# Kernel tuning notes

Hardware: AMD Instinct MI355X
Metric: run time of the kernel (lower is better)

Reference implementation:

```python
import jax, jax.numpy as jnp
import numpy as np

B, T, C, H = 1, 2048, 1024, 16
HD = C // H           # 64
TOPK = 64
RAMP = 32
MAX_SPAN = 2048
NEG_MAX = jnp.finfo(jnp.float32).max


def setup_inputs() -> dict:
    key = jax.random.key(0)
    k0, k1, k2, k3, k4 = jax.random.split(key, 5)
    x = jax.random.normal(k0, (B, T, C), jnp.float32)
    w_attn = jax.random.normal(k1, (3 * C, C), jnp.float32) * 0.02
    w_proj = jax.random.normal(k2, (C, C), jnp.float32) * 0.02
    w_gate = jax.random.normal(k3, (C, C), jnp.float32) * 0.02
    span_params = jax.random.uniform(k4, (H,), jnp.float32)
    pos = jnp.arange(T, dtype=jnp.int64) if jax.config.jax_enable_x64 else jnp.arange(T, dtype=jnp.int32)
    return {"x": x, "w_attn": w_attn, "w_proj": w_proj, "w_gate": w_gate,
            "span_params": span_params, "pos": pos}


def _rotate_half(u):
    u1, u2 = jnp.split(u, 2, axis=-1)
    return jnp.concatenate([-u2, u1], axis=-1)


def _rope(q, k):
    t = q.shape[-2]
    inv_freq = 1.0 / (10000.0 ** (jnp.arange(0, HD, 2, dtype=jnp.float32) / HD))
    freqs = jnp.arange(t, dtype=jnp.float32)[:, None] * inv_freq[None, :]  # [T, HD/2]
    emb = jnp.concatenate([freqs, freqs], axis=-1)                          # [T, HD]
    cos = jnp.cos(emb)[None, None]
    sin = jnp.sin(emb)[None, None]
    q = q * cos + _rotate_half(q * sin)
    k = k * cos + _rotate_half(k * sin)
    return q, k


def reference(x, w_attn, w_proj, w_gate, span_params, pos):
    qkv = x @ w_attn.T                                   # [B,T,3C]
    q, k, v = jnp.split(qkv, 3, axis=-1)
    q = q.reshape(B, T, H, HD).transpose(0, 2, 1, 3)     # [B,H,T,HD]
    k = k.reshape(B, T, H, HD).transpose(0, 2, 1, 3)
    v = v.reshape(B, T, H, HD).transpose(0, 2, 1, 3)
    q, k = _rope(q, k)

    att = jnp.einsum('bhqd,bhkd->bhqk', q, k) / jnp.sqrt(jnp.float32(HD))
    i = jnp.arange(T)
    causal = i[:, None] >= i[None, :]                    # [T,T]
    att = jnp.where(causal[None, None], att, -jnp.inf)

    # sparse top-k with straight-through softmax
    top_vals = jax.lax.top_k(att, TOPK)[0]               # [B,H,T,K]
    thresh = top_vals[..., -1:]
    keep = (att >= thresh) & (att > -NEG_MAX)
    att_topk = jnp.where(keep, att, -NEG_MAX)
    topk_attn = jax.nn.softmax(att_topk, axis=-1)
    soft_attn = jax.nn.softmax(att, axis=-1)
    att = jax.lax.stop_gradient(topk_attn) + soft_attn - jax.lax.stop_gradient(soft_attn)

    # adaptive span soft mask + renormalize
    spans = MAX_SPAN * jnp.clip(span_params, 0.0, 1.0)   # [H]
    dist = jnp.abs(i[:, None] - i[None, :]).astype(jnp.float32)  # [T,T]
    soft_mask = jnp.clip((RAMP + spans[:, None, None] - dist[None]) / RAMP, 0.0, 1.0)  # [H,T,T]
    att = att * soft_mask[None]
    att = att / (att.sum(-1, keepdims=True) + 1e-8)

    y = jnp.einsum('bhqk,bhkd->bhqd', att, v)            # [B,H,T,HD]
    y = y.transpose(0, 2, 1, 3).reshape(B, T, C)
    gate = jax.nn.silu(x @ w_gate.T)
    y = y * gate
    y = y @ w_proj.T
    return y
```

## Files before the change

### kernel.cpp

```cpp
#include <hip/hip_runtime.h>
#include <math.h>

#define T_DIM 2048
#define C_DIM 1024
#define H_DIM 16
#define HD 64
#define TOPK_K 64
#define QTILE 8
#define LCAP 128

typedef __attribute__((ext_vector_type(8))) __bf16 bf16x8;
typedef __attribute__((ext_vector_type(4))) float f32x4;

__device__ __forceinline__ unsigned short bf16rn(float x) {
  unsigned u = __float_as_uint(x);
  return (unsigned short)((u + 0x7FFFu + ((u >> 16) & 1u)) >> 16);
}
__device__ __forceinline__ unsigned f2u(float f) {
  unsigned u = __float_as_uint(f);
  return (u & 0x80000000u) ? ~u : (u | 0x80000000u);
}
__device__ __forceinline__ float u2f(unsigned u) {
  unsigned v = (u & 0x80000000u) ? (u & 0x7FFFFFFFu) : ~u;
  return __uint_as_float(v);
}
__device__ __forceinline__ bf16x8 ld_frag(const uint4* p) {
  uint4 u = *p;
  return __builtin_bit_cast(bf16x8, u);
}
#define PAD_KEY 0x007FFFFFu

__global__ __launch_bounds__(256) void convert_all_kernel(
    const float* __restrict__ x, const float* __restrict__ wa,
    const float* __restrict__ wg, const float* __restrict__ wp,
    unsigned short* __restrict__ xh, unsigned short* __restrict__ xl,
    unsigned short* __restrict__ wqgh, unsigned short* __restrict__ wqgl,
    unsigned short* __restrict__ wph, unsigned short* __restrict__ wpl,
    float2* __restrict__ tab)
{
  const int tid = blockIdx.x * 256 + threadIdx.x;
  const int k8 = tid & 127, r = tid >> 7;
  if (r >= 7168) {
    const int e = ((r - 7168) << 7) | k8;
    const int t = e >> 5, d = e & 31;
    double invf = exp(-(double)d * (log(10000.0) / 32.0));
    double ang = (double)t * invf;
    tab[e] = make_float2((float)cos(ang), (float)sin(ang));
    return;
  }
  const float* src;
  unsigned short *Dh, *Dl;
  int srow, drow;
  if (r < 2048)      { src = x;  Dh = xh;   Dl = xl;   srow = r;        drow = r; }
  else if (r < 5120) { src = wa; Dh = wqgh; Dl = wqgl; srow = r - 2048; drow = r - 2048; }
  else if (r < 6144) { src = wg; Dh = wqgh; Dl = wqgl; srow = r - 5120; drow = r - 2048; }
  else               { src = wp; Dh = wph;  Dl = wpl;  srow = r - 6144; drow = r - 6144; }
  const float* s = src + ((size_t)srow << 10) + (k8 << 3);
  float4 a = *(const float4*)s;
  float4 b = *(const float4*)(s + 4);
  float xs[8] = {a.x, a.y, a.z, a.w, b.x, b.y, b.z, b.w};
  unsigned hi[8], lo[8];
#pragma unroll
  for (int jj = 0; jj < 8; ++jj) {
    unsigned short hb = bf16rn(xs[jj]);
    hi[jj] = hb;
    lo[jj] = bf16rn(xs[jj] - __uint_as_float((unsigned)hb << 16));
  }
  const int t16 = drow >> 4, rr = drow & 15, kc = k8 >> 2, kq = k8 & 3;
  const size_t elem = (((size_t)(t16 * 32 + kc)) * 64 + ((kq << 4) | rr)) * 8;
  uint4 vh, vl;
  vh.x = hi[0] | (hi[1] << 16); vh.y = hi[2] | (hi[3] << 16);
  vh.z = hi[4] | (hi[5] << 16); vh.w = hi[6] | (hi[7] << 16);
  vl.x = lo[0] | (lo[1] << 16); vl.y = lo[2] | (lo[3] << 16);
  vl.z = lo[4] | (lo[5] << 16); vl.w = lo[6] | (lo[7] << 16);
  *(uint4*)(Dh + elem) = vh;
  *(uint4*)(Dl + elem) = vl;
}

__device__ __forceinline__ void gld_lds16(const unsigned short* g, unsigned short* l) {
  __builtin_amdgcn_global_load_lds(
      (const __attribute__((address_space(1))) unsigned int*)g,
      (__attribute__((address_space(3))) unsigned int*)l, 16, 0, 0);
}

__global__ __launch_bounds__(512, 4) void mgemm_qkvg_kernel(
    const unsigned short* __restrict__ Ah, const unsigned short* __restrict__ Al,
    const unsigned short* __restrict__ Bh, const unsigned short* __restrict__ Bl,
    float* __restrict__ Cq, float* __restrict__ Ck, float* __restrict__ Cv,
    float* __restrict__ Cg)
{
  __shared__ __align__(16) unsigned short As[2 * 8 * 512];
  __shared__ __align__(16) unsigned short Bs[2 * 8 * 512];
  const int tid = threadIdx.x, lane = tid & 63, w = tid >> 6;
  const int mt0 = blockIdx.y << 3;
  const int nt0 = blockIdx.x << 3;

  f32x4 acc[8];
#pragma unroll
  for (int j = 0; j < 8; ++j) acc[j] = (f32x4){0.f, 0.f, 0.f, 0.f};

  for (int kc = 0; kc < 32; ++kc) {
#pragma unroll
    for (int li = 0; li < 4; ++li) {
      const int gi = (w << 2) + li;
      const int isB = gi >= 16;
      const int gb = gi & 15;
      const int t  = gb & 7;
      const int hl = gb >> 3;
      const unsigned short* gbase = isB ? (hl ? Bl : Bh) : (hl ? Al : Ah);
      const int tg = (isB ? nt0 : mt0) + t;
      const unsigned short* g = gbase + (((size_t)(tg * 32 + kc) << 6) + lane) * 8;
      unsigned short* l = (isB ? Bs : As) + hl * 4096 + t * 512;
      gld_lds16(g, l);
    }
    __syncthreads();
    bf16x8 ah = *(const bf16x8*)&As[w * 512 + lane * 8];
    bf16x8 al = *(const bf16x8*)&As[4096 + w * 512 + lane * 8];
#pragma unroll
    for (int j = 0; j < 8; ++j) {
      bf16x8 bh = *(const bf16x8*)&Bs[j * 512 + lane * 8];
      bf16x8 bl = *(const bf16x8*)&Bs[4096 + j * 512 + lane * 8];
      acc[j] = __builtin_amdgcn_mfma_f32_16x16x32_bf16(ah, bh, acc[j], 0, 0, 0);
      acc[j] = __builtin_amdgcn_mfma_f32_16x16x32_bf16(ah, bl, acc[j], 0, 0, 0);
      acc[j] = __builtin_amdgcn_mfma_f32_16x16x32_bf16(al, bh, acc[j], 0, 0, 0);
    }
    __syncthreads();
  }

  const int col = lane & 15, quad = lane >> 4;
  const int mbase = (blockIdx.y << 7) + (w << 4);
#pragma unroll
  for (int j = 0; j < 8; ++j) {
    const int ncol = (blockIdx.x << 7) + (j << 4);
    const int which = ncol >> 10;
    if (which < 3) {
      const int h = (ncol & 1023) >> 6;
      float* dst = (which == 0) ? Cq : (which == 1) ? Ck : Cv;
      float* base = dst + (((size_t)h * T_DIM) << 6) + (ncol & 63) + col;
#pragma unroll
      for (int reg = 0; reg < 4; ++reg) {
        const int m = mbase + quad * 4 + reg;
        base[(size_t)m << 6] = acc[j][reg];
      }
    } else {
      const int cb = (ncol & 1023) + col;
#pragma unroll
      for (int reg = 0; reg < 4; ++reg) {
        const int m = mbase + quad * 4 + reg;
        float vv = acc[j][reg];
        Cg[((size_t)m << 10) + cb] = vv / (1.f + expf(-vv));
      }
    }
  }
}

__global__ __launch_bounds__(256, 4) void mgemm_proj_kernel(
    const unsigned short* __restrict__ Ah, const unsigned short* __restrict__ Al,
    const unsigned short* __restrict__ Bh, const unsigned short* __restrict__ Bl,
    float* __restrict__ P0, float* __restrict__ P1)
{
  __shared__ __align__(16) unsigned short As[2 * 4 * 512];
  __shared__ __align__(16) unsigned short Bs[2 * 8 * 512];
  const int tid = threadIdx.x, lane = tid & 63, w = tid >> 6;
  const int mt0 = blockIdx.y << 2;
  const int nt0 = blockIdx.x << 3;
  const int kc0 = blockIdx.z << 4;
  float* Cout = blockIdx.z ? P1 : P0;

  f32x4 acc[8];
#pragma unroll
  for (int j = 0; j < 8; ++j) acc[j] = (f32x4){0.f, 0.f, 0.f, 0.f};

  for (int kc = kc0; kc < kc0 + 16; ++kc) {
#pragma unroll
    for (int li = 0; li < 6; ++li) {
      const int gi = w * 6 + li;
      const int isB = gi >= 8;
      const int t  = isB ? ((gi - 8) & 7) : (gi & 3);
      const int hl = isB ? ((gi - 8) >> 3) : (gi >> 2);
      const unsigned short* gbase = isB ? (hl ? Bl : Bh) : (hl ? Al : Ah);
      const int tg = (isB ? nt0 : mt0) + t;
      const unsigned short* g = gbase + (((size_t)(tg * 32 + kc) << 6) + lane) * 8;
      unsigned short* l = isB ? (Bs + hl * 4096 + t * 512) : (As + hl * 2048 + t * 512);
      gld_lds16(g, l);
    }
    __syncthreads();
    bf16x8 ah = *(const bf16x8*)&As[w * 512 + lane * 8];
    bf16x8 al = *(const bf16x8*)&As[2048 + w * 512 + lane * 8];
#pragma unroll
    for (int j = 0; j < 8; ++j) {
      bf16x8 bh = *(const bf16x8*)&Bs[j * 512 + lane * 8];
      bf16x8 bl = *(const bf16x8*)&Bs[4096 + j * 512 + lane * 8];
      acc[j] = __builtin_amdgcn_mfma_f32_16x16x32_bf16(ah, bh, acc[j], 0, 0, 0);
      acc[j] = __builtin_amdgcn_mfma_f32_16x16x32_bf16(ah, bl, acc[j], 0, 0, 0);
      acc[j] = __builtin_amdgcn_mfma_f32_16x16x32_bf16(al, bh, acc[j], 0, 0, 0);
    }
    __syncthreads();
  }

  const int col = lane & 15, quad = lane >> 4;
  const int mbase = (blockIdx.y << 6) + (w << 4);
  const int nbase = blockIdx.x << 7;
#pragma unroll
  for (int j = 0; j < 8; ++j)
#pragma unroll
    for (int reg = 0; reg < 4; ++reg) {
      const int m = mbase + quad * 4 + reg;
      Cout[((size_t)m << 10) + nbase + (j << 4) + col] = acc[j][reg];
    }
}

__global__ __launch_bounds__(256) void add2_kernel(
    const float* __restrict__ P0, const float* __restrict__ P1,
    float* __restrict__ out)
{
  const int i = (blockIdx.x * 256 + threadIdx.x) << 2;
  float4 a = *(const float4*)(P0 + i);
  float4 b = *(const float4*)(P1 + i);
  float4 o = {a.x + b.x, a.y + b.y, a.z + b.z, a.w + b.w};
  *(float4*)(out + i) = o;
}

__global__ __launch_bounds__(64) void prep_frag_kernel(
    float* __restrict__ qb, float* __restrict__ kb,
    const float2* __restrict__ tab)
{
  float* buf = blockIdx.z ? kb : qb;
  const int lane = threadIdx.x;
  const int t16 = blockIdx.x, h = blockIdx.y;
  const int nr = lane & 15, quad = lane >> 4;
  const int t = (t16 << 4) + nr;
  const float* row = buf + ((size_t)(h * T_DIM + t) << 6);
  const int d0 = quad << 3;
  float4 a0 = *(const float4*)(row + d0);
  float4 a1 = *(const float4*)(row + d0 + 4);
  float4 b0 = *(const float4*)(row + 32 + d0);
  float4 b1 = *(const float4*)(row + 32 + d0 + 4);
  float x0[8] = {a0.x, a0.y, a0.z, a0.w, a1.x, a1.y, a1.z, a1.w};
  float x1[8] = {b0.x, b0.y, b0.z, b0.w, b1.x, b1.y, b1.z, b1.w};
  const float2* tb = tab + t * 32 + d0;
  unsigned short h0[8], l0[8], h1[8], l1[8];
#pragma unroll
  for (int jj = 0; jj < 8; ++jj) {
    float2 cs2 = tb[jj];
    float o0 = fmaf(x0[jj], cs2.x, -x1[jj] * cs2.y);
    float o1 = fmaf(x1[jj], cs2.x, x0[jj] * cs2.y);
    unsigned short hb = bf16rn(o0);
    h0[jj] = hb;
    l0[jj] = bf16rn(o0 - __uint_as_float((unsigned)hb << 16));
    hb = bf16rn(o1);
    h1[jj] = hb;
    l1[jj] = bf16rn(o1 - __uint_as_float((unsigned)hb << 16));
  }
  char* base = (char*)buf + (((size_t)(h * 128 + t16)) << 12);
  uint4 v;
  v.x = (unsigned)h0[0] | ((unsigned)h0[1] << 16);
  v.y = (unsigned)h0[2] | ((unsigned)h0[3] << 16);
  v.z = (unsigned)h0[4] | ((unsigned)h0[5] << 16);
  v.w = (unsigned)h0[6] | ((unsigned)h0[7] << 16);
  ((uint4*)base)[lane] = v;
  v.x = (unsigned)h1[0] | ((unsigned)h1[1] << 16);
  v.y = (unsigned)h1[2] | ((unsigned)h1[3] << 16);
  v.z = (unsigned)h1[4] | ((unsigned)h1[5] << 16);
  v.w = (unsigned)h1[6] | ((unsigned)h1[7] << 16);
  ((uint4*)(base + 1024))[lane] = v;
  v.x = (unsigned)l0[0] | ((unsigned)l0[1] << 16);
  v.y = (unsigned)l0[2] | ((unsigned)l0[3] << 16);
  v.z = (unsigned)l0[4] | ((unsigned)l0[5] << 16);
  v.w = (unsigned)l0[6] | ((unsigned)l0[7] << 16);
  ((uint4*)(base + 2048))[lane] = v;
  v.x = (unsigned)l1[0] | ((unsigned)l1[1] << 16);
  v.y = (unsigned)l1[2] | ((unsigned)l1[3] << 16);
  v.z = (unsigned)l1[4] | ((unsigned)l1[5] << 16);
  v.w = (unsigned)l1[6] | ((unsigned)l1[7] << 16);
  ((uint4*)(base + 3072))[lane] = v;
}

__global__ __launch_bounds__(512, 6) void attn_kernel(
    const float* __restrict__ qfrag, const float* __restrict__ kfrag,
    const float* __restrict__ v, const float* __restrict__ span_params,
    float* __restrict__ y)
{
  __shared__ __align__(16) char smem[QTILE * 1024 * 4];
  float* sBase = (float*)smem;
  unsigned* histB = (unsigned*)smem;
  int* listJB = (int*)(smem + 8192);
  unsigned* listUB = (unsigned*)(smem + 12288);

  const int tid = threadIdx.x;
  const int lane = tid & 63;
  const int w = tid >> 6;
  const int bx = gridDim.x - 1 - blockIdx.x;
  const int q0 = bx << 3;
  const int h = blockIdx.y;
  const int qi = q0 + w;
  const int n = qi + 1;
  const float* vh = v + (((size_t)h * T_DIM) << 6);
  const int col = lane & 15, quad = lane >> 4;

  const int qt16 = bx >> 1;
  const int rlo = (bx & 1) << 3;
  const uint4* qf = (const uint4*)((const char*)qfrag + (((size_t)(h * 128 + qt16)) << 12));
  bf16x8 Ah0 = ld_frag(qf + lane);
  bf16x8 Ah1 = ld_frag(qf + 64 + lane);
  bf16x8 Al0 = ld_frag(qf + 128 + lane);
  bf16x8 Al1 = ld_frag(qf + 192 + lane);

  unsigned uk[32];

#pragma unroll
  for (int ph = 0; ph < 2; ++ph) {
    const int tlo = ph << 6;
    const int thi = (qt16 < tlo + 63) ? qt16 : (tlo + 63);
    int tf = tlo + w;
    if (tf <= thi) {
      const uint4* kf = (const uint4*)((const char*)kfrag + (((size_t)(h * 128 + tf)) << 12));
      bf16x8 nBh0 = ld_frag(kf + lane);
      bf16x8 nBh1 = ld_frag(kf + 64 + lane);
      bf16x8 nBl0 = ld_frag(kf + 128 + lane);
      bf16x8 nBl1 = ld_frag(kf + 192 + lane);
      for (; tf <= thi; tf += 8) {
        const bf16x8 Bh0 = nBh0, Bh1 = nBh1, Bl0 = nBl0, Bl1 = nBl1;
        const int tn = (tf + 8 <= thi) ? (tf + 8) : tf;
        const uint4* kfn = (const uint4*)((const char*)kfrag + (((size_t)(h * 128 + tn)) << 12));
        nBh0 = ld_frag(kfn + lane);
        nBh1 = ld_frag(kfn + 64 + lane);
        nBl0 = ld_frag(kfn + 128 + lane);
        nBl1 = ld_frag(kfn + 192 + lane);
        f32x4 acc = {0.f, 0.f, 0.f, 0.f};
        acc = __builtin_amdgcn_mfma_f32_16x16x32_bf16(Ah0, Bh0, acc, 0, 0, 0);
        acc = __builtin_amdgcn_mfma_f32_16x16x32_bf16(Ah0, Bl0, acc, 0, 0, 0);
        acc = __builtin_amdgcn_mfma_f32_16x16x32_bf16(Al0, Bh0, acc, 0, 0, 0);
        acc = __builtin_amdgcn_mfma_f32_16x16x32_bf16(Ah1, Bh1, acc, 0, 0, 0);
        acc = __builtin_amdgcn_mfma_f32_16x16x32_bf16(Ah1, Bl1, acc, 0, 0, 0);
        acc = __builtin_amdgcn_mfma_f32_16x16x32_bf16(Al1, Bh1, acc, 0, 0, 0);
        const int jcol = (tf << 4) + col;
#pragma unroll
        for (int r = 0; r < 4; ++r) {
          const int row8 = (quad << 2) + r - rlo;
          if ((unsigned)row8 < 8u && jcol <= q0 + row8)
            sBase[row8 * 1024 + ((jcol & 1023) ^ (((row8 >> 2) & 1) << 4))] = acc[r];
        }
      }
    }
    __syncthreads();
#pragma unroll
    for (int cc = 0; cc < 2; ++cc) {
      const int c = (ph << 1) + cc;
      if ((c << 9) < n) {
#pragma unroll
        for (int i = 0; i < 8; ++i) {
          const int j = (((c << 3) + i) << 6) + lane;
          uk[(c << 3) + i] = (j < n)
              ? f2u(sBase[w * 1024 + ((j & 1023) ^ (((w >> 2) & 1) << 4))]) : PAD_KEY;
        }
      } else {
#pragma unroll
        for (int i = 0; i < 8; ++i) uk[(c << 3) + i] = PAD_KEY;
      }
    }
    __syncthreads();
  }

  unsigned* hist = histB + (w << 8);
  int* listJ = listJB + (w << 7);
  unsigned* listU = listUB + (w << 7);
  const float span = 2048.f * fminf(fmaxf(span_params[h], 0.f), 1.f);

  unsigned umax = 0;
#pragma unroll
  for (int i = 0; i < 32; ++i) umax = max(umax, uk[i]);
#pragma unroll
  for (int off = 32; off > 0; off >>= 1)
    umax = max(umax, (unsigned)__shfl_xor((int)umax, off, 64));
  const float mraw = u2f(umax);

  unsigned thresh_u = 0;
  if (n > TOPK_K) {
    unsigned want = TOPK_K;
    const unsigned bmax = umax >> 24;
    unsigned long long c01 = 0;
#pragma unroll
    for (int c = 0; c < 4; ++c) {
      if ((c << 9) < n) {
#pragma unroll
        for (int i = 0; i < 8; ++i) {
          const unsigned u = uk[(c << 3) + i];
          const unsigned d = bmax - (u >> 24);
          if (u > PAD_KEY && d < 4u) c01 += 1ull << (d << 4);
        }
      }
    }
#pragma unroll
    for (int off = 32; off > 0; off >>= 1)
      c01 += __shfl_xor(c01, off, 64);
    unsigned cnt8[8];
    cnt8[0] = (unsigned)c01 & 0xFFFFu;
    cnt8[1] = ((unsigned)c01) >> 16;
    cnt8[2] = (unsigned)(c01 >> 32) & 0xFFFFu;
    cnt8[3] = (unsigned)(c01 >> 48);
    int m = -1;
    unsigned cumBefore = 0;
    bool exact = false;
    unsigned cum = 0;
#pragma unroll
    for (int b = 0; b < 4; ++b) {
      if (m < 0 && cum + cnt8[b] >= want) {
        m = b; cumBefore = cum; exact = (cum + cnt8[b] == want);
      }
      cum += cnt8[b];
    }
    if (m < 0) {
      unsigned long long c23 = 0;
#pragma unroll
      for (int c = 0; c < 4; ++c) {
        if ((c << 9) < n) {
#pragma unroll
          for (int i = 0; i < 8; ++i) {
            const unsigned u = uk[(c << 3) + i];
            const unsigned d = bmax - (u >> 24) - 4u;
            if (u > PAD_KEY && d < 4u) c23 += 1ull << (d << 4);
          }
        }
      }
#pragma unroll
      for (int off = 32; off > 0; off >>= 1)
        c23 += __shfl_xor(c23, off, 64);
      cnt8[4] = (unsigned)c23 & 0xFFFFu;
      cnt8[5] = ((unsigned)c23) >> 16;
      cnt8[6] = (unsigned)(c23 >> 32) & 0xFFFFu;
      cnt8[7] = (unsigned)(c23 >> 48);
#pragma unroll
      for (int b = 4; b < 8; ++b) {
        if (m < 0 && cum + cnt8[b] >= want) {
          m = b; cumBefore = cum; exact = (cum + cnt8[b] == want);
        }
        cum += cnt8[b];
      }
    }
    unsigned prefix;
    int shift0;
    if (m >= 0) { prefix = (bmax - (unsigned)m) << 24; want -= cumBefore; shift0 = 16; }
    else        { prefix = 0; shift0 = 24; }
    if (m >= 0 && exact) {
      thresh_u = prefix;
    } else {
      for (int shift = shift0; shift >= 0; shift -= 8) {
        uint4 z4 = {0u, 0u, 0u, 0u};
        *(uint4*)&hist[lane << 2] = z4;
        __threadfence_block();
        const unsigned pm = (shift == 24) ? 0u : (0xFFFFFFFFu << (shift + 8));
#pragma unroll
        for (int c = 0; c < 4; ++c) {
          if ((c << 9) < n) {
#pragma unroll
            for (int i = 0; i < 8; ++i) {
              const unsigned u = uk[(c << 3) + i];
              if (u > PAD_KEY && (u & pm) == prefix)
                atomicAdd(&hist[(u >> shift) & 255u], 1u);
            }
          }
        }
        __threadfence_block();
        uint4 hv = *(const uint4*)&hist[lane << 2];
        unsigned loc = hv.x + hv.y + hv.z + hv.w;
        unsigned suf = loc;
#pragma unroll
        for (int off = 1; off < 64; off <<= 1) {
          unsigned t = __shfl_down(suf, off, 64);
          suf += (lane + off < 64) ? t : 0u;
        }
        unsigned sufE = suf - loc;
        unsigned S3 = sufE + hv.w;
        unsigned S2 = S3 + hv.z;
        unsigned S1 = S2 + hv.y;
        unsigned S0 = S1 + hv.x;
        const unsigned wt = want;
        int found = 0;
        unsigned pk = 0;
        if (S0 >= wt && S1 < wt)
          { found = 1; pk = ((unsigned)(4*lane+0) << 16) | ((S0 == wt) ? 0x8000u : 0u) | (wt - S1); }
        if (S1 >= wt && S2 < wt)
          { found = 1; pk = ((unsigned)(4*lane+1) << 16) | ((S1 == wt) ? 0x8000u : 0u) | (wt - S2); }
        if (S2 >= wt && S3 < wt)
          { found = 1; pk = ((unsigned)(4*lane+2) << 16) | ((S2 == wt) ? 0x8000u : 0u) | (wt - S3); }
        if (S3 >= wt && sufE < wt)
          { found = 1; pk = ((unsigned)(4*lane+3) << 16) | ((S3 == wt) ? 0x8000u : 0u) | (wt - sufE); }
        unsigned long long mk = __ballot(found);
        int src = __ffsll(mk) - 1;
        pk = __shfl(pk, src, 64);
        prefix |= (pk >> 16) << shift;
        want = pk & 0x7FFFu;
        if (pk & 0x8000u) break;
      }
      thresh_u = prefix;
    }
  }

  int cnt_run = 0;
#pragma unroll
  for (int c = 0; c < 4; ++c) {
    if ((c << 9) < n) {
#pragma unroll
      for (int i = 0; i < 8; ++i) {
        const int j = (((c << 3) + i) << 6) + lane;
        const unsigned u = uk[(c << 3) + i];
        const bool keep = (u >= thresh_u) && (u > PAD_KEY);
        unsigned long long mb = __ballot(keep);
        if (keep) {
          int pos = cnt_run + (int)__popcll(mb & ((1ull << lane) - 1ull));
          if (pos < LCAP) { listJ[pos] = j; listU[pos] = u; }
        }
        cnt_run += (int)__popcll(mb);
      }
    }
  }
  const int cnt = min(cnt_run, LCAP);
  __threadfence_block();

  float Zl = 0.f, Ul = 0.f;
  for (int e = lane; e < cnt; e += 64) {
    const unsigned u = listU[e];
    const int j = listJ[e];
    const float wv = __expf((u2f(u) - mraw) * 0.125f);
    const float dist = (float)(qi - j);
    const float msk = fminf(fmaxf((32.f + span - dist) * (1.f / 32.f), 0.f), 1.f);
    const float wm = wv * msk;
    Zl += wv;
    Ul += wm;
    listU[e] = __float_as_uint(wm);
  }
#pragma unroll
  for (int off = 32; off > 0; off >>= 1) {
    Zl += __shfl_xor(Zl, off, 64);
    Ul += __shfl_xor(Ul, off, 64);
  }
  const float scale = 1.f / (Ul + 1e-8f * Zl);
  __threadfence_block();

  const int g = lane >> 4;
  const int d4 = col << 2;
  float4 acc4 = {0.f, 0.f, 0.f, 0.f};
  for (int e0 = 0; e0 < cnt; e0 += 16) {
    int j0 = 0, j1 = 0, j2 = 0, j3 = 0;
    float wm0 = 0.f, wm1 = 0.f, wm2 = 0.f, wm3 = 0.f;
    {
      const int e = e0 + g;
      if (e < cnt) { j0 = listJ[e]; wm0 = __uint_as_float(listU[e]); }
    }
    {
      const int e = e0 + 4 + g;
      if (e < cnt) { j1 = listJ[e]; wm1 = __uint_as_float(listU[e]); }
    }
    {
      const int e = e0 + 8 + g;
      if (e < cnt) { j2 = listJ[e]; wm2 = __uint_as_float(listU[e]); }
    }
    {
      const int e = e0 + 12 + g;
      if (e < cnt) { j3 = listJ[e]; wm3 = __uint_as_float(listU[e]); }
    }
    const float4 v0 = *(const float4*)(vh + ((size_t)j0 << 6) + d4);
    const float4 v1 = *(const float4*)(vh + ((size_t)j1 << 6) + d4);
    const float4 v2 = *(const float4*)(vh + ((size_t)j2 << 6) + d4);
    const float4 v3 = *(const float4*)(vh + ((size_t)j3 << 6) + d4);
    acc4.x = fmaf(wm0, v0.x, acc4.x);
    acc4.y = fmaf(wm0, v0.y, acc4.y);
    acc4.z = fmaf(wm0, v0.z, acc4.z);
    acc4.w = fmaf(wm0, v0.w, acc4.w);
    acc4.x = fmaf(wm1, v1.x, acc4.x);
    acc4.y = fmaf(wm1, v1.y, acc4.y);
    acc4.z = fmaf(wm1, v1.z, acc4.z);
    acc4.w = fmaf(wm1, v1.w, acc4.w);
    acc4.x = fmaf(wm2, v2.x, acc4.x);
    acc4.y = fmaf(wm2, v2.y, acc4.y);
    acc4.z = fmaf(wm2, v2.z, acc4.z);
    acc4.w = fmaf(wm2, v2.w, acc4.w);
    acc4.x = fmaf(wm3, v3.x, acc4.x);
    acc4.y = fmaf(wm3, v3.y, acc4.y);
    acc4.z = fmaf(wm3, v3.z, acc4.z);
    acc4.w = fmaf(wm3, v3.w, acc4.w);
  }
#pragma unroll
  for (int off = 16; off <= 32; off <<= 1) {
    acc4.x += __shfl_xor(acc4.x, off, 64);
    acc4.y += __shfl_xor(acc4.y, off, 64);
    acc4.z += __shfl_xor(acc4.z, off, 64);
    acc4.w += __shfl_xor(acc4.w, off, 64);
  }
  if (g == 0) {
    float4 o = {acc4.x * scale, acc4.y * scale, acc4.z * scale, acc4.w * scale};
    *(float4*)(y + ((((size_t)h * T_DIM) + qi) << 6) + d4) = o;
  }
}

__global__ __launch_bounds__(256) void gate_mul_frag_kernel(
    const float* __restrict__ y_att, const float* __restrict__ gate,
    unsigned short* __restrict__ Yh, unsigned short* __restrict__ Yl)
{
  const int tid = blockIdx.x * 256 + threadIdx.x;
  const int k8 = tid & 127, r = tid >> 7;
  const int c0 = k8 << 3;
  const int h = c0 >> 6, d0 = c0 & 63;
  const float* ya = y_att + ((size_t)(h * T_DIM + r) << 6) + d0;
  const float* ga = gate + ((size_t)r << 10) + c0;
  float4 y0 = *(const float4*)ya;
  float4 y1 = *(const float4*)(ya + 4);
  float4 g0 = *(const float4*)ga;
  float4 g1 = *(const float4*)(ga + 4);
  float p[8] = {y0.x * g0.x, y0.y * g0.y, y0.z * g0.z, y0.w * g0.w,
                y1.x * g1.x, y1.y * g1.y, y1.z * g1.z, y1.w * g1.w};
  unsigned hi[8], lo[8];
#pragma unroll
  for (int jj = 0; jj < 8; ++jj) {
    unsigned short hb = bf16rn(p[jj]);
    hi[jj] = hb;
    lo[jj] = bf16rn(p[jj] - __uint_as_float((unsigned)hb << 16));
  }
  const int t16 = r >> 4, rr = r & 15, kc = k8 >> 2, kq = k8 & 3;
  const size_t elem = (((size_t)(t16 * 32 + kc)) * 64 + ((kq << 4) | rr)) * 8;
  uint4 vh, vl;
  vh.x = hi[0] | (hi[1] << 16); vh.y = hi[2] | (hi[3] << 16);
  vh.z = hi[4] | (hi[5] << 16); vh.w = hi[6] | (hi[7] << 16);
  vl.x = lo[0] | (lo[1] << 16); vl.y = lo[2] | (lo[3] << 16);
  vl.z = lo[4] | (lo[5] << 16); vl.w = lo[6] | (lo[7] << 16);
  *(uint4*)(Yh + elem) = vh;
  *(uint4*)(Yl + elem) = vl;
}

extern "C" void kernel_launch(void* const* d_in, const int* in_sizes, int n_in,
                              void* d_out, int out_size, void* d_ws, size_t ws_size,
                              hipStream_t stream) {
  (void)in_sizes; (void)n_in; (void)out_size; (void)ws_size;
  const float* x           = (const float*)d_in[0];
  const float* w_attn      = (const float*)d_in[1];
  const float* w_proj      = (const float*)d_in[2];
  const float* w_gate      = (const float*)d_in[3];
  const float* span_params = (const float*)d_in[4];
  float* out = (float*)d_out;

  char* ws = (char*)d_ws;
  const size_t MB = 1024 * 1024;
  float* q     = (float*)(ws);
  float* k     = (float*)(ws + 8 * MB);
  float* v     = (float*)(ws + 16 * MB);
  float* gate  = (float*)(ws + 24 * MB);
  float* y_att = (float*)(ws + 32 * MB);
  unsigned short* xf_h  = (unsigned short*)(ws + 40 * MB);
  unsigned short* xf_l  = (unsigned short*)(ws + 44 * MB);
  unsigned short* wqg_h = (unsigned short*)(ws + 48 * MB);
  unsigned short* wqg_l = (unsigned short*)(ws + 56 * MB);
  unsigned short* wfp_h = (unsigned short*)(ws + 64 * MB);
  unsigned short* wfp_l = (unsigned short*)(ws + 66 * MB);
  unsigned short* ygf_h = (unsigned short*)(ws + 68 * MB);
  unsigned short* ygf_l = (unsigned short*)(ws + 72 * MB);
  float2* rope_tab = (float2*)(ws + 76 * MB);
  float* P0 = q;
  float* P1 = k;

  convert_all_kernel<<<3840, 256, 0, stream>>>(
      x, w_attn, w_gate, w_proj, xf_h, xf_l, wqg_h, wqg_l, wfp_h, wfp_l, rope_tab);
  mgemm_qkvg_kernel<<<dim3(32, 16), 512, 0, stream>>>(
      xf_h, xf_l, wqg_h, wqg_l, q, k, v, gate);
  prep_frag_kernel<<<dim3(T_DIM / 16, H_DIM, 2), 64, 0, stream>>>(q, k, rope_tab);
  attn_kernel<<<dim3(T_DIM / QTILE, H_DIM), 512, 0, stream>>>(
      q, k, v, span_params, y_att);
  gate_mul_frag_kernel<<<T_DIM / 2, 256, 0, stream>>>(y_att, gate, ygf_h, ygf_l);
  mgemm_proj_kernel<<<dim3(8, 32, 2), 256, 0, stream>>>(
      ygf_h, ygf_l, wfp_h, wfp_l, P0, P1);
  add2_kernel<<<(T_DIM * C_DIM) / 1024, 256, 0, stream>>>(P0, P1, out);
}
```

Measured before the change: 286.5 us.

## Fuse gate multiply into attention epilogue and enlarge projection GEMM tile

The attention kernel's epilogue now multiplies by the SiLU gate and writes the split bf16 hi/lo fragments for the projection GEMM directly. This removes the separate gate_mul_frag kernel and the fp32 y_att round trip through global memory. The projection GEMM now uses 512-thread blocks covering 128 rows instead of 64, which halves the grid and doubles reuse of the B tile. The trade-off is fewer blocks in flight for the projection and narrower 8-byte scattered stores from attention.

```diff
diff --git a/kernel.cpp b/kernel.cpp
--- a/kernel.cpp
+++ b/kernel.cpp
@@ -154,15 +154,15 @@
   }
 }
 
-__global__ __launch_bounds__(256, 4) void mgemm_proj_kernel(
+__global__ __launch_bounds__(512, 4) void mgemm_proj_kernel(
     const unsigned short* __restrict__ Ah, const unsigned short* __restrict__ Al,
     const unsigned short* __restrict__ Bh, const unsigned short* __restrict__ Bl,
     float* __restrict__ P0, float* __restrict__ P1)
 {
-  __shared__ __align__(16) unsigned short As[2 * 4 * 512];
+  __shared__ __align__(16) unsigned short As[2 * 8 * 512];
   __shared__ __align__(16) unsigned short Bs[2 * 8 * 512];
   const int tid = threadIdx.x, lane = tid & 63, w = tid >> 6;
-  const int mt0 = blockIdx.y << 2;
+  const int mt0 = blockIdx.y << 3;
   const int nt0 = blockIdx.x << 3;
   const int kc0 = blockIdx.z << 4;
   float* Cout = blockIdx.z ? P1 : P0;
@@ -173,20 +173,21 @@
 
   for (int kc = kc0; kc < kc0 + 16; ++kc) {
 #pragma unroll
-    for (int li = 0; li < 6; ++li) {
-      const int gi = w * 6 + li;
-      const int isB = gi >= 8;
-      const int t  = isB ? ((gi - 8) & 7) : (gi & 3);
-      const int hl = isB ? ((gi - 8) >> 3) : (gi >> 2);
+    for (int li = 0; li < 4; ++li) {
+      const int gi = (w << 2) + li;
+      const int isB = gi >= 16;
+      const int gb = gi & 15;
+      const int t  = gb & 7;
+      const int hl = gb >> 3;
       const unsigned short* gbase = isB ? (hl ? Bl : Bh) : (hl ? Al : Ah);
       const int tg = (isB ? nt0 : mt0) + t;
       const unsigned short* g = gbase + (((size_t)(tg * 32 + kc) << 6) + lane) * 8;
-      unsigned short* l = isB ? (Bs + hl * 4096 + t * 512) : (As + hl * 2048 + t * 512);
+      unsigned short* l = (isB ? Bs : As) + hl * 4096 + t * 512;
       gld_lds16(g, l);
     }
     __syncthreads();
     bf16x8 ah = *(const bf16x8*)&As[w * 512 + lane * 8];
-    bf16x8 al = *(const bf16x8*)&As[2048 + w * 512 + lane * 8];
+    bf16x8 al = *(const bf16x8*)&As[4096 + w * 512 + lane * 8];
 #pragma unroll
     for (int j = 0; j < 8; ++j) {
       bf16x8 bh = *(const bf16x8*)&Bs[j * 512 + lane * 8];
@@ -199,7 +200,7 @@
   }
 
   const int col = lane & 15, quad = lane >> 4;
-  const int mbase = (blockIdx.y << 6) + (w << 4);
+  const int mbase = (blockIdx.y << 7) + (w << 4);
   const int nbase = blockIdx.x << 7;
 #pragma unroll
   for (int j = 0; j < 8; ++j)
@@ -279,7 +280,8 @@
 __global__ __launch_bounds__(512, 6) void attn_kernel(
     const float* __restrict__ qfrag, const float* __restrict__ kfrag,
     const float* __restrict__ v, const float* __restrict__ span_params,
-    float* __restrict__ y)
+    const float* __restrict__ gate,
+    unsigned short* __restrict__ Yh, unsigned short* __restrict__ Yl)
 {
   __shared__ __align__(16) char smem[QTILE * 1024 * 4];
   float* sBase = (float*)smem;
@@ -589,43 +591,25 @@
     acc4.w += __shfl_xor(acc4.w, off, 64);
   }
   if (g == 0) {
-    float4 o = {acc4.x * scale, acc4.y * scale, acc4.z * scale, acc4.w * scale};
-    *(float4*)(y + ((((size_t)h * T_DIM) + qi) << 6) + d4) = o;
-  }
-}
-
-__global__ __launch_bounds__(256) void gate_mul_frag_kernel(
-    const float* __restrict__ y_att, const float* __restrict__ gate,
-    unsigned short* __restrict__ Yh, unsigned short* __restrict__ Yl)
-{
-  const int tid = blockIdx.x * 256 + threadIdx.x;
-  const int k8 = tid & 127, r = tid >> 7;
-  const int c0 = k8 << 3;
-  const int h = c0 >> 6, d0 = c0 & 63;
-  const float* ya = y_att + ((size_t)(h * T_DIM + r) << 6) + d0;
-  const float* ga = gate + ((size_t)r << 10) + c0;
-  float4 y0 = *(const float4*)ya;
-  float4 y1 = *(const float4*)(ya + 4);
-  float4 g0 = *(const float4*)ga;
-  float4 g1 = *(const float4*)(ga + 4);
-  float p[8] = {y0.x * g0.x, y0.y * g0.y, y0.z * g0.z, y0.w * g0.w,
-                y1.x * g1.x, y1.y * g1.y, y1.z * g1.z, y1.w * g1.w};
-  unsigned hi[8], lo[8];
-#pragma unroll
-  for (int jj = 0; jj < 8; ++jj) {
-    unsigned short hb = bf16rn(p[jj]);
-    hi[jj] = hb;
-    lo[jj] = bf16rn(p[jj] - __uint_as_float((unsigned)hb << 16));
-  }
-  const int t16 = r >> 4, rr = r & 15, kc = k8 >> 2, kq = k8 & 3;
-  const size_t elem = (((size_t)(t16 * 32 + kc)) * 64 + ((kq << 4) | rr)) * 8;
-  uint4 vh, vl;
-  vh.x = hi[0] | (hi[1] << 16); vh.y = hi[2] | (hi[3] << 16);
-  vh.z = hi[4] | (hi[5] << 16); vh.w = hi[6] | (hi[7] << 16);
-  vl.x = lo[0] | (lo[1] << 16); vl.y = lo[2] | (lo[3] << 16);
-  vl.z = lo[4] | (lo[5] << 16); vl.w = lo[6] | (lo[7] << 16);
-  *(uint4*)(Yh + elem) = vh;
-  *(uint4*)(Yl + elem) = vl;
+    const int c0 = (h << 6) + d4;
+    const float4 gv = *(const float4*)(gate + ((size_t)qi << 10) + c0);
+    float p[4] = {acc4.x * scale * gv.x, acc4.y * scale * gv.y,
+                  acc4.z * scale * gv.z, acc4.w * scale * gv.w};
+    unsigned short ph[4], pl[4];
+#pragma unroll
+    for (int jj = 0; jj < 4; ++jj) {
+      unsigned short hb = bf16rn(p[jj]);
+      ph[jj] = hb;
+      pl[jj] = bf16rn(p[jj] - __uint_as_float((unsigned)hb << 16));
+    }
+    const int k8 = c0 >> 3;
+    const int t16 = qi >> 4, rr = qi & 15, kc = k8 >> 2, kq = k8 & 3;
+    const size_t elem = (((size_t)(t16 * 32 + kc)) * 64 + ((kq << 4) | rr)) * 8 + (d4 & 7);
+    ushort4 vh4 = {ph[0], ph[1], ph[2], ph[3]};
+    ushort4 vl4 = {pl[0], pl[1], pl[2], pl[3]};
+    *(ushort4*)(Yh + elem) = vh4;
+    *(ushort4*)(Yl + elem) = vl4;
+  }
 }
 
 extern "C" void kernel_launch(void* const* d_in, const int* in_sizes, int n_in,
@@ -645,7 +629,6 @@
   float* k     = (float*)(ws + 8 * MB);
   float* v     = (float*)(ws + 16 * MB);
   float* gate  = (float*)(ws + 24 * MB);
-  float* y_att = (float*)(ws + 32 * MB);
   unsigned short* xf_h  = (unsigned short*)(ws + 40 * MB);
   unsigned short* xf_l  = (unsigned short*)(ws + 44 * MB);
   unsigned short* wqg_h = (unsigned short*)(ws + 48 * MB);
@@ -664,9 +647,8 @@
       xf_h, xf_l, wqg_h, wqg_l, q, k, v, gate);
   prep_frag_kernel<<<dim3(T_DIM / 16, H_DIM, 2), 64, 0, stream>>>(q, k, rope_tab);
   attn_kernel<<<dim3(T_DIM / QTILE, H_DIM), 512, 0, stream>>>(
-      q, k, v, span_params, y_att);
-  gate_mul_frag_kernel<<<T_DIM / 2, 256, 0, stream>>>(y_att, gate, ygf_h, ygf_l);
-  mgemm_proj_kernel<<<dim3(8, 32, 2), 256, 0, stream>>>(
+      q, k, v, span_params, gate, ygf_h, ygf_l);
+  mgemm_proj_kernel<<<dim3(8, 16, 2), 512, 0, stream>>>(
       ygf_h, ygf_l, wfp_h, wfp_l, P0, P1);
   add2_kernel<<<(T_DIM * C_DIM) / 1024, 256, 0, stream>>>(P0, P1, out);
 }
```

Result: no change. 284.3 us (-0.8%).
